# Kernel optimization log

Measured on AMD Instinct MI355X. Metric: run time of the kernel, lower is better.

Reference implementation:

```python
import jax, jax.numpy as jnp
import numpy as np

BS, GS, D, KMAX = 256, 1024, 128, 4
VRANGE = 6.0
NEG = -1e30


def _u(key, shape, fan):
    s = 1.0 / np.sqrt(fan)
    return jax.random.uniform(key, shape, jnp.float32, -s, s)


def _gru(x, hp, Wih, Whh, bih, bhh):
    # torch.nn.GRUCell math
    gi = x @ Wih.T + bih
    gh = hp @ Whh.T + bhh
    ir, iz, inn = jnp.split(gi, 3, axis=-1)
    hr, hz, hn = jnp.split(gh, 3, axis=-1)
    r = jax.nn.sigmoid(ir + hr)
    z = jax.nn.sigmoid(iz + hz)
    n = jnp.tanh(inn + r * hn)
    return (1.0 - z) * n + z * hp


def _gather_h(h, idx):  # h [B,G,D], idx [B,1] -> [B,D]
    B, G, Dd = h.shape
    return jnp.take_along_axis(h, jnp.broadcast_to(idx[:, :, None], (B, 1, Dd)), axis=1)[:, 0]


def setup_inputs() -> dict:
    key = jax.random.key(0)
    ks = jax.random.split(key, 32)
    p = {}
    for i, n in enumerate(["K1", "K2", "K3", "K4", "Q1", "Q2", "Q3", "Q4"]):
        p["W_" + n] = _u(ks[i], (D, D), D)
    p["meta_W1"] = _u(ks[8], (8, 9), 9)
    p["meta_b1"] = _u(ks[9], (8,), 9)
    p["meta_W2"] = _u(ks[10], (2 * D, 8), 8)
    p["meta_b2"] = _u(ks[11], (2 * D,), 8)
    p["init_hidden_W"] = _u(ks[12], (D, D), D)
    p["init_hidden_b"] = _u(ks[13], (D,), D)
    p["init_query"] = _u(ks[14], (D,), D)
    for j, r in enumerate(["rnn1", "rnn2"]):
        p[r + "_Wih"] = _u(ks[15 + 4 * j], (3 * D, D), D)
        p[r + "_Whh"] = _u(ks[16 + 4 * j], (3 * D, D), D)
        p[r + "_bih"] = _u(ks[17 + 4 * j], (3 * D,), D)
        p[r + "_bhh"] = _u(ks[18 + 4 * j], (3 * D,), D)
    inp = dict(
        h=jax.random.normal(ks[24], (BS, GS, D), jnp.float32),
        context2=jax.random.normal(ks[25], (BS, 9), jnp.float32),
        rec=jax.random.randint(ks[26], (BS, GS), 0, GS),
        visited_time=jax.random.randint(ks[27], (BS, GS), 0, GS),
        last_action=jax.random.randint(ks[28], (BS, 1), 0, GS),
        fixed_action=jax.random.randint(ks[29], (BS, KMAX), 0, GS),
        k_max=KMAX,
    )
    inp.update(p)
    return inp


def reference(h, context2, rec, visited_time, last_action, fixed_action, k_max,
              W_K1, W_K2, W_K3, W_K4, W_Q1, W_Q2, W_Q3, W_Q4,
              meta_W1, meta_b1, meta_W2, meta_b2,
              init_hidden_W, init_hidden_b, init_query,
              rnn1_Wih, rnn1_Whh, rnn1_bih, rnn1_bhh,
              rnn2_Wih, rnn2_Whh, rnn2_bih, rnn2_bhh):
    bs, gs, d = h.shape
    # with_feature3: meta_linear(context2) -> [V1, V2]
    hid = jax.nn.relu(context2 @ meta_W1.T + meta_b1)
    lv = hid @ meta_W2.T + meta_b2
    V1, V2 = lv[:, :d], lv[:, d:]
    h_mean = h.mean(1)
    q1 = h_mean @ init_hidden_W.T + init_hidden_b
    q2 = q1
    input_q1 = jnp.broadcast_to(init_query[None, :], (bs, d))
    input_q2 = input_q1
    # K-projections are step-invariant; precompute (same math as in-loop linear_K)
    K1h = h @ W_K1.T
    K2h = h @ W_K2.T
    K3h = h @ W_K3.T
    K4h = h @ W_K4.T
    mask = jnp.zeros((bs, gs), bool)
    stopped = jnp.ones((bs,), bool)
    nola = jnp.full((bs, 1), -1, rec.dtype)  # next_of_last_action
    action_index = jnp.zeros((bs, k_max), rec.dtype)
    kal = jnp.zeros((bs, k_max + 1), rec.dtype)
    kar = jnp.zeros((bs, k_max), rec.dtype)
    ll = jnp.zeros((bs,), h.dtype)
    cols = jnp.arange(gs)[None, :]
    vtt = None
    for i in range(k_max):
        q1 = _gru(input_q1, q1, rnn1_Wih, rnn1_Whh, rnn1_bih, rnn1_bhh)
        q2 = _gru(input_q2, q2, rnn2_Wih, rnn2_Whh, rnn2_bih, rnn2_bhh)
        t1 = jnp.tanh(K1h + (q1 @ W_Q1.T)[:, None, :] + K3h * (q1 @ W_Q3.T)[:, None, :])
        t2 = jnp.tanh(K2h + (q2 @ W_Q2.T)[:, None, :] + K4h * (q2 @ W_Q4.T)[:, None, :])
        result = jnp.einsum('bgd,bd->bg', t1, V1) + jnp.einsum('bgd,bd->bg', t2, V2)
        logits = jnp.tanh(result) * VRANGE
        logits = jnp.where(mask, NEG, logits)
        if i == 0:
            logits = jnp.where(cols == last_action[:, :1], NEG, logits)
        action = fixed_action[:, i:i + 1]
        if i > 0:
            action = jnp.where(stopped[:, None], action_index[:, :1], action)
        logp = jax.nn.log_softmax(logits, axis=-1)
        loss_now = jnp.take_along_axis(logp, action, axis=1)[:, 0]
        ll = ll + (jnp.where(stopped, 0.0, loss_now) if i > 0 else loss_now)
        nona = jnp.take_along_axis(rec, action, axis=1)  # next_of_new_action
        a = action[:, 0]
        action_index = action_index.at[:, i].set(a)
        kal = kal.at[:, i].set(jnp.where(stopped, a, kal[:, i]))
        jprev = (i - 1) % k_max
        kar = kar.at[:, jprev].set(jnp.where(~stopped, a, kar[:, jprev]))
        kal = kal.at[:, i + 1].set(nona[:, 0])
        input_q1 = _gather_h(h, action)
        input_q2 = jnp.where(stopped[:, None], input_q1, _gather_h(h, nola % gs))
        hit = (action == nola)[:, 0]
        stopped = (stopped | hit) if i > 0 else hit
        kal = kal.at[:, i].set(jnp.where(stopped, kal[:, (i - 1) % (k_max + 1)], kal[:, i]))
        kar = kar.at[:, i].set(jnp.where(stopped, kar[:, jprev], kar[:, i]))
        if i == 0:
            vtt = (visited_time - jnp.take_along_axis(visited_time, action, axis=1)) % gs
        vtt_a = jnp.take_along_axis(vtt, action, axis=1)
        mask = vtt <= vtt_a
        if i == 0:
            mask = mask | (vtt > gs - 2)
        mask = jnp.where(stopped[:, None] & (cols == action), False, mask)
        allow = (~stopped) & (nona[:, 0] == action_index[:, 0])
        mask = jnp.where(allow[:, None] & (cols == action_index[:, :1]), False, mask)
        nola = jnp.where(stopped[:, None], jnp.array(-1, rec.dtype), nona)
    kar = kar.at[:, -1].set(jnp.where(~stopped, kal[:, -1], kar[:, -1]))
    action_all = jnp.concatenate([action_index, kal[:, :k_max], kar], axis=-1)
    return action_all, ll
```

## Files before the change

### kernel.cpp

```cpp
#include <hip/hip_runtime.h>
#include <hip/hip_bf16.h>
#include <math.h>

#define GS 1024
#define BSZ 256
#define DD 128
#define NEGV -1e30f

typedef __attribute__((ext_vector_type(8))) short bf16x8_t;
typedef __attribute__((ext_vector_type(4))) float f32x4_t;
typedef __attribute__((ext_vector_type(2))) float f32x2_t;

#define WGRU_OFF_BYTES 131072
#define WQP_OFF_BYTES  524288
#define WIHB_OFF_BYTES 655360
#define F_OFF_BYTES    688128
#define FH_HM   0
#define FI_V    262144
#define FJ_AQB  327680
#define FK_RES  851968
#define F_TOTAL 1900544
#define DESC_OFF_BYTES (F_OFF_BYTES + F_TOTAL * 4)

__device__ __forceinline__ float rtanh(float x) {
    float s = fmaf(x, x, 1.0f);
    return x * __builtin_amdgcn_rsqf(s);
}
__device__ __forceinline__ float tanh2(float x) {
    float e = __expf(x + x);
    return fmaf(-2.0f, __builtin_amdgcn_rcpf(e + 1.0f), 1.0f);
}
__device__ __forceinline__ float sigm2(float x) {
    return __builtin_amdgcn_rcpf(1.0f + __expf(-x));
}
__device__ __forceinline__ unsigned short f2bf(float f) {
    union { float f; unsigned u; } v; v.f = f;
    unsigned u = v.u;
    return (unsigned short)((u + 0x7fffu + ((u >> 16) & 1u)) >> 16);
}
#define MFMA16(a, b, c) __builtin_amdgcn_mfma_f32_16x16x32_bf16((a), (b), (c), 0, 0, 0)

__global__ __launch_bounds__(128) void init_kernel(
    const float* __restrict__ h,
    const float* __restrict__ wk1, const float* __restrict__ wk2,
    const float* __restrict__ wk3, const float* __restrict__ wk4,
    const float* __restrict__ wq1, const float* __restrict__ wq2,
    const float* __restrict__ wq3, const float* __restrict__ wq4,
    const float* __restrict__ ihw,
    const float* __restrict__ r1ih, const float* __restrict__ r1hh,
    const float* __restrict__ r2ih, const float* __restrict__ r2hh,
    unsigned short* __restrict__ wbf, unsigned short* __restrict__ wgru,
    unsigned short* __restrict__ wqp, unsigned short* __restrict__ wihb,
    float* __restrict__ F)
{
    if (blockIdx.x < 2048) {
        int b = blockIdx.x >> 3, seg = blockIdx.x & 7, d = threadIdx.x;
        const float* base = h + ((size_t)(b * GS + seg * 128)) * DD + d;
        float s = 0.0f;
#pragma unroll 8
        for (int r = 0; r < 128; r++) s += base[(size_t)r * DD];
        F[FH_HM + b * 1024 + seg * 128 + d] = s;
        return;
    }
    int tid = (blockIdx.x - 2048) * 128 + threadIdx.x;
    int nth = 128 * 128;
    const float* wks[4]  = {wk1, wk2, wk3, wk4};
    const float* rws[4]  = {r1ih, r1hh, r2ih, r2hh};
    const float* wqs2[4] = {wq1, wq3, wq2, wq4};

    for (int e = tid; e < 65536; e += nth)
        wbf[e] = f2bf(wks[e >> 14][e & 16383]);
    for (int e = tid; e < 196608; e += nth)
        wgru[e] = f2bf(rws[e / 49152][e % 49152]);
    for (int e = tid; e < 65536; e += nth)
        wqp[e] = f2bf(wqs2[e >> 14][e & 16383]);
    for (int e = tid; e < 16384; e += nth)
        wihb[e] = f2bf(ihw[e]);
}

__global__ __launch_bounds__(512) void prep_kernel(
    const float* __restrict__ h, const float* __restrict__ ctx2,
    const int* __restrict__ rec, const int* __restrict__ vt,
    const int* __restrict__ la_, const int* __restrict__ fa,
    const float* __restrict__ mW1, const float* __restrict__ mb1,
    const float* __restrict__ mW2, const float* __restrict__ mb2,
    const float* __restrict__ ihb, const float* __restrict__ iq,
    const float* __restrict__ b1ih, const float* __restrict__ b1hh,
    const float* __restrict__ b2ih, const float* __restrict__ b2hh,
    const unsigned short* __restrict__ wgru, const unsigned short* __restrict__ wqp,
    const unsigned short* __restrict__ wihb,
    float* __restrict__ F, int* __restrict__ DESC, float* __restrict__ out)
{
    int rho = blockIdx.x & 1;
    int b0  = (blockIdx.x >> 1) * 16;
    int t = threadIdx.x;
    int lane = t & 63, w = t >> 6, ml = lane & 15, quad = lane >> 4;
    int dloc = w * 16 + ml;

    __shared__ __attribute__((aligned(16))) unsigned short hmb[16][136];
    __shared__ __attribute__((aligned(16))) unsigned short Xall[4][16][136];
    __shared__ __attribute__((aligned(16))) unsigned short Qb[2][16][136];
    __shared__ float hid[16][8];
    __shared__ int sdesc[16][26];

    const float* bih = rho ? b2ih : b1ih;
    const float* bhh = rho ? b2hh : b1hh;

#pragma unroll
    for (int k = 0; k < 4; k++) {
        int e = t + 512 * k;
        int b = e >> 7, d = e & 127;
        float s = 0.0f;
#pragma unroll
        for (int seg = 0; seg < 8; seg++)
            s += F[FH_HM + (b0 + b) * 1024 + seg * 128 + d];
        hmb[b][d] = f2bf(s * (1.0f / 1024.0f));
    }
    if (t < 128) {
        int b = t >> 3, u = t & 7;
        float a = mb1[u];
        for (int k = 0; k < 9; k++) a += mW1[u * 9 + k] * ctx2[(b0 + b) * 9 + k];
        hid[b][u] = a > 0.0f ? a : 0.0f;
    }
    if (t >= 128 && t < 144) {
        int tb = t - 128;
        int b = b0 + tb;
        int ai[4], kal[5] = {0, 0, 0, 0, 0}, kar[4] = {0, 0, 0, 0};
        int idesc[26];
        int stopped = 1, nola = -1, vt0 = 0;
        for (int i = 0; i < 4; i++) {
            idesc[16 + i] = stopped;
            idesc[22 + i] = nola;
            int action = fa[b * 4 + i];
            if (i > 0 && stopped) action = ai[0];
            int nona = rec[b * GS + action];
            ai[i] = action;
            if (stopped) kal[i] = action;
            int jprev = (i + 3) & 3;
            if (!stopped) kar[jprev] = action;
            kal[i + 1] = nona;
            int hit = (action == nola) ? 1 : 0;
            int st = (i > 0) ? (stopped | hit) : hit;
            if (st) kal[i] = kal[(i + 4) % 5];
            if (st) kar[i] = kar[jprev];
            if (i == 0) vt0 = vt[b * GS + action];
            idesc[0 + i]  = action;
            idesc[4 + i]  = (vt[b * GS + action] - vt0) & (GS - 1);
            idesc[8 + i]  = st;
            idesc[12 + i] = (!st && (nona == ai[0])) ? 1 : 0;
            nola = st ? -1 : nona;
            stopped = st;
        }
        if (!stopped) kar[3] = kal[4];
        idesc[20] = la_[b];
        idesc[21] = vt0;
        int* dd = DESC + b * 32;
        for (int c = 0; c < 26; c++) { dd[c] = idesc[c]; sdesc[tb][c] = idesc[c]; }
        float* oa = out + b * 12;
        for (int c = 0; c < 4; c++) {
            oa[c]     = (float)ai[c];
            oa[4 + c] = (float)kal[c];
            oa[8 + c] = (float)kar[c];
        }
    }
    __syncthreads();

#pragma unroll
    for (int k = 0; k < 8; k++) {
        int o = t + 512 * k;
        int b = o >> 8, idx = o & 255;
        float a = mb2[idx];
#pragma unroll
        for (int u = 0; u < 8; u++) a += mW2[idx * 8 + u] * hid[b][u];
        F[FI_V + (b0 + b) * 256 + idx] = a;
    }
    for (int e = t; e < 2048; e += 512) {
        int row = e >> 7, d = e & 127;
        Xall[0][row][d] = f2bf(iq[d]);
    }
    for (int e = t; e < 6144; e += 512) {
        int i = (e >> 11) + 1;
        int b = (e >> 7) & 15, d = e & 127;
        int a = sdesc[b][i - 1];
        int srcrow = a;
        if (rho) {
            int sE = sdesc[b][16 + (i - 1)];
            int nl = sdesc[b][22 + (i - 1)];
            srcrow = sE ? a : (nl & (GS - 1));
        }
        Xall[i][b][d] = f2bf(h[((size_t)((b0 + b) * GS + srcrow)) * DD + d]);
    }
    float qreg[4];
    {
        bf16x8_t am[4];
#pragma unroll
        for (int kt = 0; kt < 4; kt++)
            am[kt] = *(const bf16x8_t*)&hmb[ml][kt * 32 + quad * 8];
        const unsigned short* wb = wihb + (size_t)dloc * 128 + quad * 8;
        f32x4_t acc = {0.f, 0.f, 0.f, 0.f};
#pragma unroll
        for (int kt = 0; kt < 4; kt++)
            acc = MFMA16(am[kt], *(const bf16x8_t*)(wb + kt * 32), acc);
        float bias = ihb[dloc];
#pragma unroll
        for (int r_ = 0; r_ < 4; r_++) {
            qreg[r_] = acc[r_] + bias;
            Qb[0][quad * 4 + r_][dloc] = f2bf(qreg[r_]);
        }
    }
    __syncthreads();

    float bir = bih[dloc], biz = bih[128 + dloc], bin_ = bih[256 + dloc];
    float bhr = bhh[dloc], bhz = bhh[128 + dloc], bhn = bhh[256 + dloc];

    for (int i = 0; i < 4; i++) {
        int cur = i & 1;
        bf16x8_t ax[4], aq[4];
#pragma unroll
        for (int kt = 0; kt < 4; kt++) {
            ax[kt] = *(const bf16x8_t*)&Xall[i][ml][kt * 32 + quad * 8];
            aq[kt] = *(const bf16x8_t*)&Qb[cur][ml][kt * 32 + quad * 8];
        }
        f32x4_t gi[3], gh[3];
#pragma unroll
        for (int gate = 0; gate < 3; gate++) {
            int n = gate * 128 + dloc;
            const unsigned short* wi = wgru + ((size_t)((rho * 2 + 0) * 384 + n)) * 128 + quad * 8;
            const unsigned short* wh = wgru + ((size_t)((rho * 2 + 1) * 384 + n)) * 128 + quad * 8;
            f32x4_t ai = {0.f, 0.f, 0.f, 0.f}, ah = {0.f, 0.f, 0.f, 0.f};
#pragma unroll
            for (int kt = 0; kt < 4; kt++) {
                ai = MFMA16(ax[kt], *(const bf16x8_t*)(wi + kt * 32), ai);
                ah = MFMA16(aq[kt], *(const bf16x8_t*)(wh + kt * 32), ah);
            }
            gi[gate] = ai; gh[gate] = ah;
        }
#pragma unroll
        for (int r_ = 0; r_ < 4; r_++) {
            float r = sigm2(gi[0][r_] + bir + gh[0][r_] + bhr);
            float z = sigm2(gi[1][r_] + biz + gh[1][r_] + bhz);
            float n = tanh2(gi[2][r_] + bin_ + r * (gh[2][r_] + bhn));
            qreg[r_] = fmaf(z, qreg[r_] - n, n);
            Qb[cur ^ 1][quad * 4 + r_][dloc] = f2bf(qreg[r_]);
        }
        __syncthreads();

        bf16x8_t aqn[4];
#pragma unroll
        for (int kt = 0; kt < 4; kt++)
            aqn[kt] = *(const bf16x8_t*)&Qb[cur ^ 1][ml][kt * 32 + quad * 8];
#pragma unroll
        for (int half = 0; half < 2; half++) {
            int nrow = half * 128 + dloc;
            const unsigned short* wq = wqp + ((size_t)(rho * 256 + nrow)) * 128 + quad * 8;
            f32x4_t acc = {0.f, 0.f, 0.f, 0.f};
#pragma unroll
            for (int kt = 0; kt < 4; kt++)
                acc = MFMA16(aqn[kt], *(const bf16x8_t*)(wq + kt * 32), acc);
            int sel = rho * 2 + half;
#pragma unroll
            for (int r_ = 0; r_ < 4; r_++) {
                int b2 = b0 + quad * 4 + r_;
                F[FJ_AQB + b2 * 2048 + dloc * 16 + i * 4 + sel] = acc[r_];
            }
        }
    }
}

#define SROW 136
__global__ __launch_bounds__(512, 4) void score_kernel(
    const float* __restrict__ h, const unsigned short* __restrict__ wbf,
    float* __restrict__ F)
{
    int b = blockIdx.x >> 1, gh = blockIdx.x & 1;
    int t = threadIdx.x;
    int lane = t & 63, w = t >> 6;
    int ml = lane & 15, quad = lane >> 4;
    int dg = w * 16 + ml;

    __shared__ __attribute__((aligned(16))) unsigned short stg[2][16 * SROW];
    __shared__ float red[2][64];

    bf16x8_t bfr[4][4];
#pragma unroll
    for (int mat = 0; mat < 4; mat++)
#pragma unroll
        for (int kt = 0; kt < 4; kt++)
            bfr[mat][kt] = *(const bf16x8_t*)(wbf + ((size_t)(mat * 128 + dg)) * 128 + kt * 32 + quad * 8);
#pragma unroll
    for (int mat = 0; mat < 4; mat++)
#pragma unroll
        for (int kt = 0; kt < 4; kt++)
            asm volatile("" : "+v"(bfr[mat][kt]));

    const float* Vb = F + FI_V + b * 256;
    f32x2_t VV = {Vb[dg], Vb[128 + dg]};
    const float* AQ = F + FJ_AQB + b * 2048 + dg * 16;
    f32x2_t aa[4], bb[4];
#pragma unroll
    for (int j = 0; j < 4; j++) {
        f32x4_t q = *(const f32x4_t*)(AQ + j * 4);
        aa[j] = (f32x2_t){q[0], q[2]};
        bb[j] = (f32x2_t){q[1], q[3]};
    }

    int srow = t >> 5;
    int scol = (t & 31) * 4;
    const float* hbase = h + ((size_t)(b * GS + gh * 512 + srow)) * DD + scol;

    if (t < 128) red[t >> 6][t & 63] = 0.0f;

    f32x4_t pre = *(const f32x4_t*)hbase;
    {
        uint2 pk;
        pk.x = (unsigned)f2bf(pre[0]) | ((unsigned)f2bf(pre[1]) << 16);
        pk.y = (unsigned)f2bf(pre[2]) | ((unsigned)f2bf(pre[3]) << 16);
        *(uint2*)&stg[0][srow * SROW + scol] = pk;
    }
    __syncthreads();

    for (int tl = 0; tl < 32; tl++) {
        if (tl + 1 < 32)
            pre = *(const f32x4_t*)(hbase + (size_t)(tl + 1) * 16 * DD);

        const unsigned short* sb = stg[tl & 1];
        f32x4_t c[4];
#pragma unroll
        for (int mat = 0; mat < 4; mat++) c[mat] = (f32x4_t){0.f, 0.f, 0.f, 0.f};
#pragma unroll
        for (int kt = 0; kt < 4; kt++) {
            bf16x8_t af = *(const bf16x8_t*)(sb + ml * SROW + kt * 32 + quad * 8);
#pragma unroll
            for (int mat = 0; mat < 4; mat++)
                c[mat] = MFMA16(af, bfr[mat][kt], c[mat]);
        }
        float v[16];
#pragma unroll
        for (int r = 0; r < 4; r++) {
            f32x2_t cA = {c[0][r], c[1][r]};
            f32x2_t cM = {c[2][r], c[3][r]};
#pragma unroll
            for (int j = 0; j < 4; j++) {
                f32x2_t y = cA + aa[j] + cM * bb[j];
                f32x2_t s = y * y + (f32x2_t){1.0f, 1.0f};
                f32x2_t rs = {__builtin_amdgcn_rsqf(s[0]), __builtin_amdgcn_rsqf(s[1])};
                f32x2_t tv = y * rs * VV;
                v[r * 4 + j] = tv[0] + tv[1];
            }
        }
        {
            int bs = ml & 1;
#pragma unroll
            for (int i = 0; i < 8; i++) {
                float lo = v[2 * i], hi = v[2 * i + 1];
                float send = bs ? lo : hi;
                float recv = __shfl_xor(send, 1);
                v[i] = (bs ? hi : lo) + recv;
            }
        }
        {
            int bs = (ml >> 1) & 1;
#pragma unroll
            for (int i = 0; i < 4; i++) {
                float lo = v[2 * i], hi = v[2 * i + 1];
                float send = bs ? lo : hi;
                float recv = __shfl_xor(send, 2);
                v[i] = (bs ? hi : lo) + recv;
            }
        }
        {
            int bs = (ml >> 2) & 1;
#pragma unroll
            for (int i = 0; i < 2; i++) {
                float lo = v[2 * i], hi = v[2 * i + 1];
                float send = bs ? lo : hi;
                float recv = __shfl_xor(send, 4);
                v[i] = (bs ? hi : lo) + recv;
            }
        }
        {
            int bs = (ml >> 3) & 1;
            float lo = v[0], hi = v[1];
            float send = bs ? lo : hi;
            float recv = __shfl_xor(send, 8);
            v[0] = (bs ? hi : lo) + recv;
        }
        atomicAdd(&red[tl & 1][quad * 16 + ml], v[0]);

        if (tl + 1 < 32) {
            uint2 pk;
            pk.x = (unsigned)f2bf(pre[0]) | ((unsigned)f2bf(pre[1]) << 16);
            pk.y = (unsigned)f2bf(pre[2]) | ((unsigned)f2bf(pre[3]) << 16);
            *(uint2*)&stg[(tl + 1) & 1][srow * SROW + scol] = pk;
        }
        __syncthreads();
        if (t < 64) {
            int j = t >> 4, gp = t & 15;
            int ridx = (gp >> 2) * 16 + (gp & 3) * 4 + j;
            float val = red[tl & 1][ridx];
            red[tl & 1][ridx] = 0.0f;
            int g = gh * 512 + tl * 16 + gp;
            F[FK_RES + (size_t)b * 4096 + j * 1024 + g] = val;
        }
    }
}

__global__ __launch_bounds__(256) void finalize_kernel(
    const float* __restrict__ F, const int* __restrict__ DESC,
    const int* __restrict__ vt, float* __restrict__ out)
{
    int b = blockIdx.x, t = threadIdx.x;
    const int* dd = DESC + b * 32;
    int act0 = dd[0], la = dd[20], vt0 = dd[21];
    __shared__ float sred[8];
    __shared__ float schosen;
    float ll = 0.0f;

    int vtts[4];
#pragma unroll
    for (int q = 0; q < 4; q++) {
        int g = t + q * 256;
        vtts[q] = (vt[b * GS + g] - vt0) & (GS - 1);
    }

    for (int j = 0; j < 4; j++) {
        int aj = dd[j];
        float lg[4];
#pragma unroll
        for (int q = 0; q < 4; q++) {
            int g = t + q * 256;
            bool neg;
            if (j == 0) {
                neg = (g == la);
            } else {
                int p = j - 1;
                neg = (vtts[q] <= dd[4 + p]) || (p == 0 && vtts[q] > GS - 2);
                if (dd[8 + p] && g == dd[p]) neg = false;
                if (dd[12 + p] && g == act0) neg = false;
            }
            float r = F[FK_RES + (size_t)b * 4096 + j * 1024 + g];
            float vv = neg ? NEGV : 6.0f * rtanh(r);
            lg[q] = vv;
            if (g == aj) schosen = vv;
        }
        float mx = fmaxf(fmaxf(lg[0], lg[1]), fmaxf(lg[2], lg[3]));
#pragma unroll
        for (int o = 1; o < 64; o <<= 1) mx = fmaxf(mx, __shfl_xor(mx, o));
        if ((t & 63) == 0) sred[t >> 6] = mx;
        __syncthreads();
        mx = fmaxf(fmaxf(sred[0], sred[1]), fmaxf(sred[2], sred[3]));
        float sm = 0.0f;
#pragma unroll
        for (int q = 0; q < 4; q++) sm += __expf(lg[q] - mx);
#pragma unroll
        for (int o = 1; o < 64; o <<= 1) sm += __shfl_xor(sm, o);
        if ((t & 63) == 0) sred[4 + (t >> 6)] = sm;
        __syncthreads();
        if (t == 0) {
            float tot = sred[4] + sred[5] + sred[6] + sred[7];
            float lse = mx + logf(tot);
            int gate = (j == 0) || (!dd[16 + j]);
            if (gate) ll += schosen - lse;
        }
        __syncthreads();
    }
    if (t == 0) out[3072 + b] = ll;
}

extern "C" void kernel_launch(void* const* d_in, const int* in_sizes, int n_in,
                              void* d_out, int out_size, void* d_ws, size_t ws_size,
                              hipStream_t stream)
{
    (void)in_sizes; (void)n_in; (void)out_size; (void)ws_size;
    const float* h    = (const float*)d_in[0];
    const float* ctx2 = (const float*)d_in[1];
    const int*   rec  = (const int*)d_in[2];
    const int*   vtm  = (const int*)d_in[3];
    const int*   la   = (const int*)d_in[4];
    const int*   fa   = (const int*)d_in[5];
    const float* wk1 = (const float*)d_in[7];
    const float* wk2 = (const float*)d_in[8];
    const float* wk3 = (const float*)d_in[9];
    const float* wk4 = (const float*)d_in[10];
    const float* wq1 = (const float*)d_in[11];
    const float* wq2 = (const float*)d_in[12];
    const float* wq3 = (const float*)d_in[13];
    const float* wq4 = (const float*)d_in[14];
    const float* mW1 = (const float*)d_in[15];
    const float* mb1 = (const float*)d_in[16];
    const float* mW2 = (const float*)d_in[17];
    const float* mb2 = (const float*)d_in[18];
    const float* ihw = (const float*)d_in[19];
    const float* ihb = (const float*)d_in[20];
    const float* iq  = (const float*)d_in[21];
    const float* r1ih = (const float*)d_in[22];
    const float* r1hh = (const float*)d_in[23];
    const float* b1ih = (const float*)d_in[24];
    const float* b1hh = (const float*)d_in[25];
    const float* r2ih = (const float*)d_in[26];
    const float* r2hh = (const float*)d_in[27];
    const float* b2ih = (const float*)d_in[28];
    const float* b2hh = (const float*)d_in[29];

    unsigned short* wbf  = (unsigned short*)d_ws;
    unsigned short* wgru = (unsigned short*)((char*)d_ws + WGRU_OFF_BYTES);
    unsigned short* wqp  = (unsigned short*)((char*)d_ws + WQP_OFF_BYTES);
    unsigned short* wihb = (unsigned short*)((char*)d_ws + WIHB_OFF_BYTES);
    float* F   = (float*)((char*)d_ws + F_OFF_BYTES);
    int* DESC  = (int*)((char*)d_ws + DESC_OFF_BYTES);
    float* out = (float*)d_out;

    init_kernel<<<dim3(2176), dim3(128), 0, stream>>>(h, wk1, wk2, wk3, wk4,
                                                      wq1, wq2, wq3, wq4, ihw,
                                                      r1ih, r1hh, r2ih, r2hh,
                                                      wbf, wgru, wqp, wihb, F);
    prep_kernel<<<dim3(32), dim3(512), 0, stream>>>(h, ctx2, rec, vtm, la, fa,
                                                    mW1, mb1, mW2, mb2, ihb, iq,
                                                    b1ih, b1hh, b2ih, b2hh,
                                                    wgru, wqp, wihb, F, DESC, out);
    score_kernel<<<dim3(512), dim3(512), 0, stream>>>(h, wbf, F);
    finalize_kernel<<<dim3(256), dim3(256), 0, stream>>>(F, DESC, vtm, out);
}
```

Before: 405.0 us.

## Convert h to bf16 once in init and load MFMA operands directly in score

The init pass that already streams h for row sums now also writes a bf16 copy of h to workspace, provided the workspace is large enough. The score kernel then loads MFMA A-fragments straight from global memory, reading bf16 or converting fp32 in registers, instead of staging through double-buffered shared memory with a barrier per tile. Each block covers a quarter of a batch row and defers writing results until the end, with double-buffered register prefetch. This trades an extra 64MB write plus a re-read for the removal of per-tile syncs and halves the bytes score reads, but occupancy is lowered to 2 blocks per SIMD pair.

```diff
diff --git a/kernel.cpp b/kernel.cpp
--- a/kernel.cpp
+++ b/kernel.cpp
@@ -21,6 +21,8 @@
 #define FK_RES  851968
 #define F_TOTAL 1900544
 #define DESC_OFF_BYTES (F_OFF_BYTES + F_TOTAL * 4)
+#define HBF_OFF_BYTES  (DESC_OFF_BYTES + 32768)
+#define WS_NEED ((size_t)HBF_OFF_BYTES + (size_t)BSZ * GS * DD * 2)
 
 __device__ __forceinline__ float rtanh(float x) {
     float s = fmaf(x, x, 1.0f);
@@ -51,14 +53,25 @@
     const float* __restrict__ r2ih, const float* __restrict__ r2hh,
     unsigned short* __restrict__ wbf, unsigned short* __restrict__ wgru,
     unsigned short* __restrict__ wqp, unsigned short* __restrict__ wihb,
-    float* __restrict__ F)
+    float* __restrict__ F, unsigned short* __restrict__ hbf, int use_hbf)
 {
     if (blockIdx.x < 2048) {
         int b = blockIdx.x >> 3, seg = blockIdx.x & 7, d = threadIdx.x;
-        const float* base = h + ((size_t)(b * GS + seg * 128)) * DD + d;
+        size_t rowbase = (size_t)(b * GS + seg * 128);
+        const float* base = h + rowbase * DD + d;
         float s = 0.0f;
+        if (use_hbf) {
+            unsigned short* ob = hbf + rowbase * DD + d;
 #pragma unroll 8
-        for (int r = 0; r < 128; r++) s += base[(size_t)r * DD];
+            for (int r = 0; r < 128; r++) {
+                float v = base[(size_t)r * DD];
+                s += v;
+                ob[(size_t)r * DD] = f2bf(v);
+            }
+        } else {
+#pragma unroll 8
+            for (int r = 0; r < 128; r++) s += base[(size_t)r * DD];
+        }
         F[FH_HM + b * 1024 + seg * 128 + d] = s;
         return;
     }
@@ -267,19 +280,81 @@
     }
 }
 
-#define SROW 136
-__global__ __launch_bounds__(512, 4) void score_kernel(
-    const float* __restrict__ h, const unsigned short* __restrict__ wbf,
-    float* __restrict__ F)
+#define LOADA(dst, TL) do {                                                    \
+    if (HBF) {                                                                 \
+        _Pragma("unroll")                                                      \
+        for (int kt = 0; kt < 4; kt++)                                         \
+            dst[kt] = *(const bf16x8_t*)(ab + (size_t)(TL) * 2048 + kt * 32);  \
+    } else {                                                                   \
+        _Pragma("unroll")                                                      \
+        for (int kt = 0; kt < 4; kt++) {                                       \
+            f32x4_t lo = *(const f32x4_t*)(fb + (size_t)(TL) * 2048 + kt * 32);     \
+            f32x4_t hi = *(const f32x4_t*)(fb + (size_t)(TL) * 2048 + kt * 32 + 4); \
+            union { unsigned short s[8]; bf16x8_t v; } pk_;                    \
+            pk_.s[0] = f2bf(lo[0]); pk_.s[1] = f2bf(lo[1]);                    \
+            pk_.s[2] = f2bf(lo[2]); pk_.s[3] = f2bf(lo[3]);                    \
+            pk_.s[4] = f2bf(hi[0]); pk_.s[5] = f2bf(hi[1]);                    \
+            pk_.s[6] = f2bf(hi[2]); pk_.s[7] = f2bf(hi[3]);                    \
+            dst[kt] = pk_.v;                                                   \
+        }                                                                      \
+    }                                                                          \
+} while (0)
+
+#define COMPUTE(TL, af) do {                                                   \
+    f32x4_t c[4];                                                              \
+    _Pragma("unroll") for (int m_ = 0; m_ < 4; m_++)                           \
+        c[m_] = (f32x4_t){0.f, 0.f, 0.f, 0.f};                                 \
+    _Pragma("unroll") for (int kt = 0; kt < 4; kt++) {                         \
+        _Pragma("unroll") for (int m_ = 0; m_ < 4; m_++)                       \
+            c[m_] = MFMA16(af[kt], bfr[m_][kt], c[m_]);                        \
+    }                                                                          \
+    float v[16];                                                               \
+    _Pragma("unroll") for (int r_ = 0; r_ < 4; r_++) {                         \
+        f32x2_t cA = {c[0][r_], c[1][r_]};                                     \
+        f32x2_t cM = {c[2][r_], c[3][r_]};                                     \
+        _Pragma("unroll") for (int j_ = 0; j_ < 4; j_++) {                     \
+            f32x2_t y = cA + aa[j_] + cM * bb[j_];                             \
+            f32x2_t s = y * y + (f32x2_t){1.0f, 1.0f};                         \
+            f32x2_t rs = {__builtin_amdgcn_rsqf(s[0]), __builtin_amdgcn_rsqf(s[1])}; \
+            f32x2_t tv = y * rs * VV;                                          \
+            v[r_ * 4 + j_] = tv[0] + tv[1];                                    \
+        }                                                                      \
+    }                                                                          \
+    { int bs = ml & 1;                                                         \
+      _Pragma("unroll") for (int i_ = 0; i_ < 8; i_++) {                       \
+          float lo = v[2 * i_], hi = v[2 * i_ + 1];                            \
+          float send = bs ? lo : hi; float recv = __shfl_xor(send, 1);         \
+          v[i_] = (bs ? hi : lo) + recv; } }                                   \
+    { int bs = (ml >> 1) & 1;                                                  \
+      _Pragma("unroll") for (int i_ = 0; i_ < 4; i_++) {                       \
+          float lo = v[2 * i_], hi = v[2 * i_ + 1];                            \
+          float send = bs ? lo : hi; float recv = __shfl_xor(send, 2);         \
+          v[i_] = (bs ? hi : lo) + recv; } }                                   \
+    { int bs = (ml >> 2) & 1;                                                  \
+      _Pragma("unroll") for (int i_ = 0; i_ < 2; i_++) {                       \
+          float lo = v[2 * i_], hi = v[2 * i_ + 1];                            \
+          float send = bs ? lo : hi; float recv = __shfl_xor(send, 4);         \
+          v[i_] = (bs ? hi : lo) + recv; } }                                   \
+    { int bs = (ml >> 3) & 1;                                                  \
+      float lo = v[0], hi = v[1];                                              \
+      float send = bs ? lo : hi; float recv = __shfl_xor(send, 8);             \
+      v[0] = (bs ? hi : lo) + recv; }                                          \
+    atomicAdd(&red[TL][quad * 16 + ml], v[0]);                                 \
+} while (0)
+
+template<int HBF>
+__global__ __launch_bounds__(512, 2) void score_kernel(
+    const float* __restrict__ h, const unsigned short* __restrict__ hbf,
+    const unsigned short* __restrict__ wbf, float* __restrict__ F)
 {
-    int b = blockIdx.x >> 1, gh = blockIdx.x & 1;
+    int b = blockIdx.x >> 2, gq = blockIdx.x & 3;
     int t = threadIdx.x;
     int lane = t & 63, w = t >> 6;
     int ml = lane & 15, quad = lane >> 4;
     int dg = w * 16 + ml;
 
-    __shared__ __attribute__((aligned(16))) unsigned short stg[2][16 * SROW];
-    __shared__ float red[2][64];
+    __shared__ float red[16][64];
+    for (int e = t; e < 1024; e += 512) ((float*)red)[e] = 0.0f;
 
     bf16x8_t bfr[4][4];
 #pragma unroll
@@ -304,104 +379,28 @@
         bb[j] = (f32x2_t){q[1], q[3]};
     }
 
-    int srow = t >> 5;
-    int scol = (t & 31) * 4;
-    const float* hbase = h + ((size_t)(b * GS + gh * 512 + srow)) * DD + scol;
-
-    if (t < 128) red[t >> 6][t & 63] = 0.0f;
-
-    f32x4_t pre = *(const f32x4_t*)hbase;
-    {
-        uint2 pk;
-        pk.x = (unsigned)f2bf(pre[0]) | ((unsigned)f2bf(pre[1]) << 16);
-        pk.y = (unsigned)f2bf(pre[2]) | ((unsigned)f2bf(pre[3]) << 16);
-        *(uint2*)&stg[0][srow * SROW + scol] = pk;
-    }
     __syncthreads();
 
-    for (int tl = 0; tl < 32; tl++) {
-        if (tl + 1 < 32)
-            pre = *(const f32x4_t*)(hbase + (size_t)(tl + 1) * 16 * DD);
-
-        const unsigned short* sb = stg[tl & 1];
-        f32x4_t c[4];
-#pragma unroll
-        for (int mat = 0; mat < 4; mat++) c[mat] = (f32x4_t){0.f, 0.f, 0.f, 0.f};
-#pragma unroll
-        for (int kt = 0; kt < 4; kt++) {
-            bf16x8_t af = *(const bf16x8_t*)(sb + ml * SROW + kt * 32 + quad * 8);
-#pragma unroll
-            for (int mat = 0; mat < 4; mat++)
-                c[mat] = MFMA16(af, bfr[mat][kt], c[mat]);
-        }
-        float v[16];
-#pragma unroll
-        for (int r = 0; r < 4; r++) {
-            f32x2_t cA = {c[0][r], c[1][r]};
-            f32x2_t cM = {c[2][r], c[3][r]};
-#pragma unroll
-            for (int j = 0; j < 4; j++) {
-                f32x2_t y = cA + aa[j] + cM * bb[j];
-                f32x2_t s = y * y + (f32x2_t){1.0f, 1.0f};
-                f32x2_t rs = {__builtin_amdgcn_rsqf(s[0]), __builtin_amdgcn_rsqf(s[1])};
-                f32x2_t tv = y * rs * VV;
-                v[r * 4 + j] = tv[0] + tv[1];
-            }
-        }
-        {
-            int bs = ml & 1;
-#pragma unroll
-            for (int i = 0; i < 8; i++) {
-                float lo = v[2 * i], hi = v[2 * i + 1];
-                float send = bs ? lo : hi;
-                float recv = __shfl_xor(send, 1);
-                v[i] = (bs ? hi : lo) + recv;
-            }
-        }
-        {
-            int bs = (ml >> 1) & 1;
-#pragma unroll
-            for (int i = 0; i < 4; i++) {
-                float lo = v[2 * i], hi = v[2 * i + 1];
-                float send = bs ? lo : hi;
-                float recv = __shfl_xor(send, 2);
-                v[i] = (bs ? hi : lo) + recv;
-            }
-        }
-        {
-            int bs = (ml >> 2) & 1;
-#pragma unroll
-            for (int i = 0; i < 2; i++) {
-                float lo = v[2 * i], hi = v[2 * i + 1];
-                float send = bs ? lo : hi;
-                float recv = __shfl_xor(send, 4);
-                v[i] = (bs ? hi : lo) + recv;
-            }
-        }
-        {
-            int bs = (ml >> 3) & 1;
-            float lo = v[0], hi = v[1];
-            float send = bs ? lo : hi;
-            float recv = __shfl_xor(send, 8);
-            v[0] = (bs ? hi : lo) + recv;
-        }
-        atomicAdd(&red[tl & 1][quad * 16 + ml], v[0]);
-
-        if (tl + 1 < 32) {
-            uint2 pk;
-            pk.x = (unsigned)f2bf(pre[0]) | ((unsigned)f2bf(pre[1]) << 16);
-            pk.y = (unsigned)f2bf(pre[2]) | ((unsigned)f2bf(pre[3]) << 16);
-            *(uint2*)&stg[(tl + 1) & 1][srow * SROW + scol] = pk;
-        }
-        __syncthreads();
-        if (t < 64) {
-            int j = t >> 4, gp = t & 15;
-            int ridx = (gp >> 2) * 16 + (gp & 3) * 4 + j;
-            float val = red[tl & 1][ridx];
-            red[tl & 1][ridx] = 0.0f;
-            int g = gh * 512 + tl * 16 + gp;
-            F[FK_RES + (size_t)b * 4096 + j * 1024 + g] = val;
-        }
+    int grow0 = gq * 256;
+    const unsigned short* ab = hbf + ((size_t)(b * GS + grow0) + ml) * 128 + quad * 8;
+    const float*          fb = h   + ((size_t)(b * GS + grow0) + ml) * 128 + quad * 8;
+
+    bf16x8_t afA[4], afB[4];
+    LOADA(afA, 0);
+#pragma unroll
+    for (int tp = 0; tp < 8; tp++) {
+        LOADA(afB, 2 * tp + 1);
+        COMPUTE(2 * tp, afA);
+        if (tp < 7) LOADA(afA, 2 * tp + 2);
+        COMPUTE(2 * tp + 1, afB);
+    }
+    __syncthreads();
+
+    for (int e = t; e < 1024; e += 512) {
+        int j = e >> 8, gl = e & 255;
+        int tl = gl >> 4, row = gl & 15;
+        float val = red[tl][(row >> 2) * 16 + (row & 3) * 4 + j];
+        F[FK_RES + (size_t)b * 4096 + j * 1024 + grow0 + gl] = val;
     }
 }
 
@@ -471,7 +470,7 @@
                               void* d_out, int out_size, void* d_ws, size_t ws_size,
                               hipStream_t stream)
 {
-    (void)in_sizes; (void)n_in; (void)out_size; (void)ws_size;
+    (void)in_sizes; (void)n_in; (void)out_size;
     const float* h    = (const float*)d_in[0];
     const float* ctx2 = (const float*)d_in[1];
     const int*   rec  = (const int*)d_in[2];
@@ -508,16 +507,23 @@
     unsigned short* wihb = (unsigned short*)((char*)d_ws + WIHB_OFF_BYTES);
     float* F   = (float*)((char*)d_ws + F_OFF_BYTES);
     int* DESC  = (int*)((char*)d_ws + DESC_OFF_BYTES);
+    unsigned short* hbf = (unsigned short*)((char*)d_ws + HBF_OFF_BYTES);
     float* out = (float*)d_out;
+
+    int use_hbf = (ws_size >= WS_NEED) ? 1 : 0;
 
     init_kernel<<<dim3(2176), dim3(128), 0, stream>>>(h, wk1, wk2, wk3, wk4,
                                                       wq1, wq2, wq3, wq4, ihw,
                                                       r1ih, r1hh, r2ih, r2hh,
-                                                      wbf, wgru, wqp, wihb, F);
+                                                      wbf, wgru, wqp, wihb, F,
+                                                      hbf, use_hbf);
     prep_kernel<<<dim3(32), dim3(512), 0, stream>>>(h, ctx2, rec, vtm, la, fa,
                                                     mW1, mb1, mW2, mb2, ihb, iq,
                                                     b1ih, b1hh, b2ih, b2hh,
                                                     wgru, wqp, wihb, F, DESC, out);
-    score_kernel<<<dim3(512), dim3(512), 0, stream>>>(h, wbf, F);
+    if (use_hbf)
+        score_kernel<1><<<dim3(1024), dim3(512), 0, stream>>>(h, hbf, wbf, F);
+    else
+        score_kernel<0><<<dim3(1024), dim3(512), 0, stream>>>(h, hbf, wbf, F);
     finalize_kernel<<<dim3(256), dim3(256), 0, stream>>>(F, DESC, vtm, out);
 }
```

New measurement: 424.2 us. 1.05x slower.
